# Kernel tuning notes

Measured on AMD Instinct MI355X. Metric: run time of the kernel, lower is better.

The kernel has to match this reference:

```python
import jax, jax.numpy as jnp
import numpy as np
import math

# Fixed ChunkedBlockDiagonalMask configuration (int metadata, closed over)
BATCH_SIZES = [32, 16, 8]
SEQ_LENS = [512, 1024, 2048]
NUM_HEADS = 8
HEAD_DIM = 64
TOTAL_TOKENS = sum(b * s for b, s in zip(BATCH_SIZES, SEQ_LENS))  # 49152


def setup_inputs() -> dict:
    key = jax.random.key(0)
    kq, kk, kv = jax.random.split(key, 3)
    shape = (1, NUM_HEADS, TOTAL_TOKENS, HEAD_DIM)
    return {
        "query": jax.random.normal(kq, shape, dtype=jnp.float32),
        "key": jax.random.normal(kk, shape, dtype=jnp.float32),
        "value": jax.random.normal(kv, shape, dtype=jnp.float32),
    }


def _sdpa(q, k, v):
    # q,k,v: [B, H, S, D]; native-backend math: softmax(q k^T / sqrt(D)) v
    scale = 1.0 / math.sqrt(q.shape[-1])
    scores = jnp.einsum("bhqd,bhkd->bhqk", q * scale, k)
    probs = jax.nn.softmax(scores, axis=-1)
    return jnp.einsum("bhqk,bhkd->bhqd", probs, v)


def reference(query, key, value):
    # Packed layout: [1, H, sum_i(B_i*S_i), D]; per-chunk token dim is (B_i S_i)
    H, D = query.shape[1], query.shape[3]
    outs = []
    offset = 0
    for b, s in zip(BATCH_SIZES, SEQ_LENS):
        n = b * s
        def unpack(t):
            # [1,H,(b s),D] -> [b,H,s,D]
            c = t[0, :, offset:offset + n, :]          # [H, b*s, D]
            return c.reshape(H, b, s, D).transpose(1, 0, 2, 3)
        o = _sdpa(unpack(query), unpack(key), unpack(value))  # [b,H,s,D]
        outs.append(o.transpose(1, 0, 2, 3).reshape(1, H, n, D))
        offset += n
    return jnp.concatenate(outs, axis=2)
```

## Files before the change

### kernel.cpp

```cpp
#include <hip/hip_runtime.h>

typedef __bf16 bf16_t;
typedef bf16_t bf16x8 __attribute__((ext_vector_type(8)));
typedef float f32x16 __attribute__((ext_vector_type(16)));
typedef unsigned short u16x8_t __attribute__((ext_vector_type(8)));
typedef unsigned int u32x4_t __attribute__((ext_vector_type(4)));

#define HD 64
#define TOTTOK 49152

static __device__ __forceinline__ unsigned short f2b(float f) {
    bf16_t h = (bf16_t)f;
    return __builtin_bit_cast(unsigned short, h);
}
static __device__ __forceinline__ bf16x8 asbf(u16x8_t u) { return __builtin_bit_cast(bf16x8, u); }
static __device__ __forceinline__ bf16x8 asbf4(u32x4_t u) { return __builtin_bit_cast(bf16x8, u); }
static __device__ __forceinline__ unsigned int pk2(float lo, float hi) {
    return (unsigned int)f2b(lo) | ((unsigned int)f2b(hi) << 16);
}

__global__ __launch_bounds__(256, 2)
void flash_attn_kernel(const float* __restrict__ Q, const float* __restrict__ K,
                       const float* __restrict__ V, float* __restrict__ O)
{
    __shared__ unsigned short Kf[2][4096];
    __shared__ unsigned short Vff[2][4096];

    const int bid = blockIdx.x;
    int Slen, bl2, off, qtl2, base;
    if (bid < 512)       { Slen = 2048; bl2 = 3; off = 32768; qtl2 = 3; base = 0;    }
    else if (bid < 1024) { Slen = 1024; bl2 = 4; off = 16384; qtl2 = 2; base = 512;  }
    else                 { Slen = 512;  bl2 = 5; off = 0;     qtl2 = 1; base = 1024; }
    const int l    = bid - base;
    const int xcd  = l & 7;
    const int slot = l >> 3;
    const int p    = xcd + ((slot >> qtl2) << 3);
    const int qblk = slot & ((1 << qtl2) - 1);
    const int hh   = p >> bl2;
    const int sj   = p & ((1 << bl2) - 1);

    const size_t seqbase = ((size_t)hh * TOTTOK + (size_t)off + (size_t)sj * Slen) * HD;
    const float* Qb = Q + seqbase + (size_t)(qblk * 256) * HD;
    const float* Kb = K + seqbase;
    const float* Vb = V + seqbase;
    float*       Ob = O + seqbase + (size_t)(qblk * 256) * HD;

    const int tid  = threadIdx.x;
    const int wave = tid >> 6;
    const int lane = tid & 63;
    const int l31  = lane & 31;
    const int hl   = lane >> 5;

    const float SC = 0.125f * 1.4426950408889634f;

    bf16x8 qf[2][4];
#pragma unroll
    for (int qt = 0; qt < 2; ++qt)
#pragma unroll
      for (int kk = 0; kk < 4; ++kk) {
        const float* src = Qb + (size_t)(wave*64 + qt*32 + l31) * HD + kk*16 + hl*8;
        float4 a = *(const float4*)src;
        float4 b = *(const float4*)(src + 4);
        float f[8] = {a.x,a.y,a.z,a.w,b.x,b.y,b.z,b.w};
        bf16x8 v;
#pragma unroll
        for (int i = 0; i < 8; ++i) v[i] = (bf16_t)(f[i] * SC);
        qf[qt][kk] = v;
      }

    f32x16 oacc[2][2];
    f32x16 lacc[2];
#pragma unroll
    for (int i = 0; i < 16; ++i) {
      oacc[0][0][i] = 0.f; oacc[0][1][i] = 0.f;
      oacc[1][0][i] = 0.f; oacc[1][1][i] = 0.f;
      lacc[0][i] = 0.f;    lacc[1][i] = 0.f;
    }

    u16x8_t onesu;
#pragma unroll
    for (int i = 0; i < 8; ++i) onesu[i] = 0x3F80;
    const bf16x8 ones = asbf(onesu);

    const int krow = tid & 31;
    const int kcol = ((tid >> 6) & 3) * 16 + ((tid >> 5) & 1) * 8;
    const int vkey = ((tid >> 6) & 3) * 16 + ((tid >> 5) & 1) * 8;
    const int vd   = tid & 31;

    float4 kr0, kr1, kr2, kr3;
    float vra[8], vrb[8];

    auto LOADT = [&](int it) {
      const float* Ksrc = Kb + (size_t)(it * 64) * HD;
      const float* Vsrc = Vb + (size_t)(it * 64) * HD;
      kr0 = *(const float4*)(Ksrc + (size_t)krow * HD + kcol);
      kr1 = *(const float4*)(Ksrc + (size_t)krow * HD + kcol + 4);
      kr2 = *(const float4*)(Ksrc + (size_t)(krow + 32) * HD + kcol);
      kr3 = *(const float4*)(Ksrc + (size_t)(krow + 32) * HD + kcol + 4);
#pragma unroll
      for (int i = 0; i < 8; ++i) {
        vra[i] = Vsrc[(size_t)(vkey + i) * HD + vd];
        vrb[i] = Vsrc[(size_t)(vkey + i) * HD + vd + 32];
      }
    };
    auto STORET = [&](int buf) {
      u16x8_t a;
      a[0]=f2b(kr0.x); a[1]=f2b(kr0.y); a[2]=f2b(kr0.z); a[3]=f2b(kr0.w);
      a[4]=f2b(kr1.x); a[5]=f2b(kr1.y); a[6]=f2b(kr1.z); a[7]=f2b(kr1.w);
      *(u16x8_t*)&Kf[buf][tid*8] = a;
      a[0]=f2b(kr2.x); a[1]=f2b(kr2.y); a[2]=f2b(kr2.z); a[3]=f2b(kr2.w);
      a[4]=f2b(kr3.x); a[5]=f2b(kr3.y); a[6]=f2b(kr3.z); a[7]=f2b(kr3.w);
      *(u16x8_t*)&Kf[buf][2048 + tid*8] = a;
      u16x8_t b;
#pragma unroll
      for (int i = 0; i < 8; ++i) b[i] = f2b(vra[i]);
      *(u16x8_t*)&Vff[buf][tid*8] = b;
#pragma unroll
      for (int i = 0; i < 8; ++i) b[i] = f2b(vrb[i]);
      *(u16x8_t*)&Vff[buf][2048 + tid*8] = b;
    };

    const int niter = Slen >> 6;
    LOADT(0);
    STORET(0);
    __syncthreads();

    for (int it = 0; it < niter; ++it) {
      const int cur = it & 1;
      const bool more = (it + 1 < niter);
      if (more) LOADT(it + 1);

      bf16x8 kf[8];
#pragma unroll
      for (int c2 = 0; c2 < 8; ++c2)
        kf[c2] = asbf(*(const u16x8_t*)&Kf[cur][c2*512 + lane*8]);

      u32x4_t pb[2][4];
#pragma unroll
      for (int qt = 0; qt < 2; ++qt) {
        f32x16 s0, s1;
#pragma unroll
        for (int i = 0; i < 16; ++i) { s0[i] = 0.f; s1[i] = 0.f; }
        __builtin_amdgcn_s_setprio(1);
#pragma unroll
        for (int kk = 0; kk < 4; ++kk) {
          s0 = __builtin_amdgcn_mfma_f32_32x32x16_bf16(kf[kk],     qf[qt][kk], s0, 0, 0, 0);
          s1 = __builtin_amdgcn_mfma_f32_32x32x16_bf16(kf[4 + kk], qf[qt][kk], s1, 0, 0, 0);
        }
        __builtin_amdgcn_s_setprio(0);
#pragma unroll
        for (int kt = 0; kt < 2; ++kt) {
          const f32x16& s = kt ? s1 : s0;
#pragma unroll
          for (int m = 0; m < 2; ++m) {
            unsigned int w0 = pk2(__builtin_amdgcn_exp2f(s[8*m+0]), __builtin_amdgcn_exp2f(s[8*m+1]));
            unsigned int w1 = pk2(__builtin_amdgcn_exp2f(s[8*m+2]), __builtin_amdgcn_exp2f(s[8*m+3]));
            unsigned int w2 = pk2(__builtin_amdgcn_exp2f(s[8*m+4]), __builtin_amdgcn_exp2f(s[8*m+5]));
            unsigned int w3 = pk2(__builtin_amdgcn_exp2f(s[8*m+6]), __builtin_amdgcn_exp2f(s[8*m+7]));
            asm("v_permlane32_swap_b32 %0, %1" : "+v"(w0), "+v"(w2));
            asm("v_permlane32_swap_b32 %0, %1" : "+v"(w1), "+v"(w3));
            pb[qt][2*kt + m] = (u32x4_t){w0, w1, w2, w3};
          }
        }
      }

      bf16x8 vf[8];
#pragma unroll
      for (int c2 = 0; c2 < 8; ++c2)
        vf[c2] = asbf(*(const u16x8_t*)&Vff[cur][c2*512 + lane*8]);

      __builtin_amdgcn_s_setprio(1);
#pragma unroll
      for (int kk4 = 0; kk4 < 4; ++kk4) {
        bf16x8 p0 = asbf4(pb[0][kk4]);
        bf16x8 p1 = asbf4(pb[1][kk4]);
        lacc[0] = __builtin_amdgcn_mfma_f32_32x32x16_bf16(ones, p0, lacc[0], 0, 0, 0);
        lacc[1] = __builtin_amdgcn_mfma_f32_32x32x16_bf16(ones, p1, lacc[1], 0, 0, 0);
        oacc[0][0] = __builtin_amdgcn_mfma_f32_32x32x16_bf16(vf[kk4],     p0, oacc[0][0], 0, 0, 0);
        oacc[0][1] = __builtin_amdgcn_mfma_f32_32x32x16_bf16(vf[kk4],     p1, oacc[0][1], 0, 0, 0);
        oacc[1][0] = __builtin_amdgcn_mfma_f32_32x32x16_bf16(vf[4 + kk4], p0, oacc[1][0], 0, 0, 0);
        oacc[1][1] = __builtin_amdgcn_mfma_f32_32x32x16_bf16(vf[4 + kk4], p1, oacc[1][1], 0, 0, 0);
      }
      __builtin_amdgcn_s_setprio(0);

      if (more) {
        STORET(cur ^ 1);
        __syncthreads();
      }
    }

#pragma unroll
    for (int qt = 0; qt < 2; ++qt) {
      float inv = 1.0f / lacc[qt][0];
      float* dst = Ob + (size_t)(wave*64 + qt*32 + l31) * HD + hl*4;
#pragma unroll
      for (int dt = 0; dt < 2; ++dt)
#pragma unroll
        for (int b = 0; b < 4; ++b) {
          float4 o4;
          o4.x = oacc[dt][qt][4*b+0] * inv;
          o4.y = oacc[dt][qt][4*b+1] * inv;
          o4.z = oacc[dt][qt][4*b+2] * inv;
          o4.w = oacc[dt][qt][4*b+3] * inv;
          *(float4*)(dst + dt*32 + b*8) = o4;
        }
    }
}

extern "C" void kernel_launch(void* const* d_in, const int* in_sizes, int n_in,
                              void* d_out, int out_size, void* d_ws, size_t ws_size,
                              hipStream_t stream) {
    (void)in_sizes; (void)n_in; (void)out_size; (void)d_ws; (void)ws_size;
    const float* Q = (const float*)d_in[0];
    const float* K = (const float*)d_in[1];
    const float* V = (const float*)d_in[2];
    float* O = (float*)d_out;
    flash_attn_kernel<<<dim3(1536), dim3(256), 0, stream>>>(Q, K, V, O);
}
```

Measured before the change: 198.4 us.

## Pipeline QK softmax with previous PV and compute row sums in VALU

Restructures the main loop so the QK^T and exp of the next key tile are issued alongside the PV MFMAs of the previous tile, using a triple-buffered V tile in shared memory. Row sums of the probabilities are accumulated in fp32 registers with one cross-half shuffle at the end, replacing the ones-vector MFMAs. This removes a third of the PV MFMAs and aims to overlap exp/VALU work with matrix work. It raises register pressure from the extra probability buffer and LDS use from the third V buffer. The sum now uses unrounded exps rather than the bf16 values used in PV.

```diff
diff --git a/kernel.cpp b/kernel.cpp
--- a/kernel.cpp
+++ b/kernel.cpp
@@ -24,7 +24,7 @@
                        const float* __restrict__ V, float* __restrict__ O)
 {
     __shared__ unsigned short Kf[2][4096];
-    __shared__ unsigned short Vff[2][4096];
+    __shared__ unsigned short Vff[3][4096];
 
     const int bid = blockIdx.x;
     int Slen, bl2, off, qtl2, base;
@@ -69,18 +69,12 @@
       }
 
     f32x16 oacc[2][2];
-    f32x16 lacc[2];
+    float lsum[2] = {0.f, 0.f};
 #pragma unroll
     for (int i = 0; i < 16; ++i) {
       oacc[0][0][i] = 0.f; oacc[0][1][i] = 0.f;
       oacc[1][0][i] = 0.f; oacc[1][1][i] = 0.f;
-      lacc[0][i] = 0.f;    lacc[1][i] = 0.f;
     }
-
-    u16x8_t onesu;
-#pragma unroll
-    for (int i = 0; i < 8; ++i) onesu[i] = 0x3F80;
-    const bf16x8 ones = asbf(onesu);
 
     const int krow = tid & 31;
     const int kcol = ((tid >> 6) & 3) * 16 + ((tid >> 5) & 1) * 8;
@@ -103,39 +97,32 @@
         vrb[i] = Vsrc[(size_t)(vkey + i) * HD + vd + 32];
       }
     };
-    auto STORET = [&](int buf) {
+    auto STORET = [&](int tile, int vbuf) {
+      unsigned short* kd = &Kf[tile & 1][0];
       u16x8_t a;
       a[0]=f2b(kr0.x); a[1]=f2b(kr0.y); a[2]=f2b(kr0.z); a[3]=f2b(kr0.w);
       a[4]=f2b(kr1.x); a[5]=f2b(kr1.y); a[6]=f2b(kr1.z); a[7]=f2b(kr1.w);
-      *(u16x8_t*)&Kf[buf][tid*8] = a;
+      *(u16x8_t*)(kd + tid*8) = a;
       a[0]=f2b(kr2.x); a[1]=f2b(kr2.y); a[2]=f2b(kr2.z); a[3]=f2b(kr2.w);
       a[4]=f2b(kr3.x); a[5]=f2b(kr3.y); a[6]=f2b(kr3.z); a[7]=f2b(kr3.w);
-      *(u16x8_t*)&Kf[buf][2048 + tid*8] = a;
+      *(u16x8_t*)(kd + 2048 + tid*8) = a;
+      unsigned short* vdst = &Vff[vbuf][0];
       u16x8_t b;
 #pragma unroll
       for (int i = 0; i < 8; ++i) b[i] = f2b(vra[i]);
-      *(u16x8_t*)&Vff[buf][tid*8] = b;
+      *(u16x8_t*)(vdst + tid*8) = b;
 #pragma unroll
       for (int i = 0; i < 8; ++i) b[i] = f2b(vrb[i]);
-      *(u16x8_t*)&Vff[buf][2048 + tid*8] = b;
-    };
-
-    const int niter = Slen >> 6;
-    LOADT(0);
-    STORET(0);
-    __syncthreads();
-
-    for (int it = 0; it < niter; ++it) {
-      const int cur = it & 1;
-      const bool more = (it + 1 < niter);
-      if (more) LOADT(it + 1);
-
+      *(u16x8_t*)(vdst + 2048 + tid*8) = b;
+    };
+
+    u32x4_t pbA[2][4], pbB[2][4];
+
+    auto QKS = [&](const unsigned short* kb, u32x4_t (&pbo)[2][4]) {
       bf16x8 kf[8];
 #pragma unroll
       for (int c2 = 0; c2 < 8; ++c2)
-        kf[c2] = asbf(*(const u16x8_t*)&Kf[cur][c2*512 + lane*8]);
-
-      u32x4_t pb[2][4];
+        kf[c2] = asbf(*(const u16x8_t*)(kb + c2*512 + lane*8));
 #pragma unroll
       for (int qt = 0; qt < 2; ++qt) {
         f32x16 s0, s1;
@@ -148,50 +135,81 @@
           s1 = __builtin_amdgcn_mfma_f32_32x32x16_bf16(kf[4 + kk], qf[qt][kk], s1, 0, 0, 0);
         }
         __builtin_amdgcn_s_setprio(0);
+        float ls = 0.f;
 #pragma unroll
         for (int kt = 0; kt < 2; ++kt) {
           const f32x16& s = kt ? s1 : s0;
 #pragma unroll
           for (int m = 0; m < 2; ++m) {
-            unsigned int w0 = pk2(__builtin_amdgcn_exp2f(s[8*m+0]), __builtin_amdgcn_exp2f(s[8*m+1]));
-            unsigned int w1 = pk2(__builtin_amdgcn_exp2f(s[8*m+2]), __builtin_amdgcn_exp2f(s[8*m+3]));
-            unsigned int w2 = pk2(__builtin_amdgcn_exp2f(s[8*m+4]), __builtin_amdgcn_exp2f(s[8*m+5]));
-            unsigned int w3 = pk2(__builtin_amdgcn_exp2f(s[8*m+6]), __builtin_amdgcn_exp2f(s[8*m+7]));
+            float e0 = __builtin_amdgcn_exp2f(s[8*m+0]), e1 = __builtin_amdgcn_exp2f(s[8*m+1]);
+            float e2 = __builtin_amdgcn_exp2f(s[8*m+2]), e3 = __builtin_amdgcn_exp2f(s[8*m+3]);
+            float e4 = __builtin_amdgcn_exp2f(s[8*m+4]), e5 = __builtin_amdgcn_exp2f(s[8*m+5]);
+            float e6 = __builtin_amdgcn_exp2f(s[8*m+6]), e7 = __builtin_amdgcn_exp2f(s[8*m+7]);
+            ls += ((e0 + e1) + (e2 + e3)) + ((e4 + e5) + (e6 + e7));
+            unsigned int w0 = pk2(e0, e1);
+            unsigned int w1 = pk2(e2, e3);
+            unsigned int w2 = pk2(e4, e5);
+            unsigned int w3 = pk2(e6, e7);
             asm("v_permlane32_swap_b32 %0, %1" : "+v"(w0), "+v"(w2));
             asm("v_permlane32_swap_b32 %0, %1" : "+v"(w1), "+v"(w3));
-            pb[qt][2*kt + m] = (u32x4_t){w0, w1, w2, w3};
+            pbo[qt][2*kt + m] = (u32x4_t){w0, w1, w2, w3};
           }
         }
-      }
-
-      bf16x8 vf[8];
-#pragma unroll
-      for (int c2 = 0; c2 < 8; ++c2)
-        vf[c2] = asbf(*(const u16x8_t*)&Vff[cur][c2*512 + lane*8]);
-
+        lsum[qt] += ls;
+      }
+    };
+
+    auto PV = [&](const u32x4_t (&pbi)[2][4], const unsigned short* vb) {
       __builtin_amdgcn_s_setprio(1);
 #pragma unroll
       for (int kk4 = 0; kk4 < 4; ++kk4) {
-        bf16x8 p0 = asbf4(pb[0][kk4]);
-        bf16x8 p1 = asbf4(pb[1][kk4]);
-        lacc[0] = __builtin_amdgcn_mfma_f32_32x32x16_bf16(ones, p0, lacc[0], 0, 0, 0);
-        lacc[1] = __builtin_amdgcn_mfma_f32_32x32x16_bf16(ones, p1, lacc[1], 0, 0, 0);
-        oacc[0][0] = __builtin_amdgcn_mfma_f32_32x32x16_bf16(vf[kk4],     p0, oacc[0][0], 0, 0, 0);
-        oacc[0][1] = __builtin_amdgcn_mfma_f32_32x32x16_bf16(vf[kk4],     p1, oacc[0][1], 0, 0, 0);
-        oacc[1][0] = __builtin_amdgcn_mfma_f32_32x32x16_bf16(vf[4 + kk4], p0, oacc[1][0], 0, 0, 0);
-        oacc[1][1] = __builtin_amdgcn_mfma_f32_32x32x16_bf16(vf[4 + kk4], p1, oacc[1][1], 0, 0, 0);
+        bf16x8 v0 = asbf(*(const u16x8_t*)(vb + kk4*512 + lane*8));
+        bf16x8 v1 = asbf(*(const u16x8_t*)(vb + (4 + kk4)*512 + lane*8));
+        bf16x8 p0 = asbf4(pbi[0][kk4]);
+        bf16x8 p1 = asbf4(pbi[1][kk4]);
+        oacc[0][0] = __builtin_amdgcn_mfma_f32_32x32x16_bf16(v0, p0, oacc[0][0], 0, 0, 0);
+        oacc[0][1] = __builtin_amdgcn_mfma_f32_32x32x16_bf16(v0, p1, oacc[0][1], 0, 0, 0);
+        oacc[1][0] = __builtin_amdgcn_mfma_f32_32x32x16_bf16(v1, p0, oacc[1][0], 0, 0, 0);
+        oacc[1][1] = __builtin_amdgcn_mfma_f32_32x32x16_bf16(v1, p1, oacc[1][1], 0, 0, 0);
       }
       __builtin_amdgcn_s_setprio(0);
-
+    };
+
+    const int niter = Slen >> 6;
+
+    LOADT(0);
+    STORET(0, 0);
+    __syncthreads();
+
+    LOADT(1);
+    QKS(&Kf[0][0], pbA);
+    STORET(1, 1);
+    __syncthreads();
+
+    int vprev = 0;
+    int vst   = 2;
+    for (int it = 1; it < niter; ++it) {
+      const bool more = (it + 1 < niter);
+      if (more) LOADT(it + 1);
+      PV(pbA, &Vff[vprev][0]);
+      QKS(&Kf[it & 1][0], pbB);
+#pragma unroll
+      for (int qt = 0; qt < 2; ++qt)
+#pragma unroll
+        for (int k = 0; k < 4; ++k) pbA[qt][k] = pbB[qt][k];
       if (more) {
-        STORET(cur ^ 1);
+        STORET(it + 1, vst);
         __syncthreads();
       }
+      vprev = (vprev == 2) ? 0 : vprev + 1;
+      vst   = (vst   == 2) ? 0 : vst   + 1;
     }
+    PV(pbA, &Vff[vprev][0]);
 
 #pragma unroll
     for (int qt = 0; qt < 2; ++qt) {
-      float inv = 1.0f / lacc[qt][0];
+      float ls = lsum[qt] + __shfl_xor(lsum[qt], 32);
+      float inv = 1.0f / ls;
       float* dst = Ob + (size_t)(wave*64 + qt*32 + l31) * HD + hl*4;
 #pragma unroll
       for (int dt = 0; dt < 2; ++dt)
```

After: 668.0 us. 3.37x slower.

## Process two 64-key tiles per barrier with split global loads

Applied to the files above, without the earlier changes.

The main loop now handles 128 keys per iteration, stored as two 64-key sub-tiles in each double-buffered LDS slot. The global loads for the next epoch are split so that each sub-tile's load is hidden behind one compute body, and there is one __syncthreads per 128 keys instead of per 64. V fragments are now read from LDS inside the PV MFMA loop instead of being preloaded, which lowers register pressure. The cost is twice the LDS footprint (32KB per block), which may affect occupancy at two blocks per CU, and a larger unrolled body.

```diff
diff --git a/kernel.cpp b/kernel.cpp
--- a/kernel.cpp
+++ b/kernel.cpp
@@ -19,12 +19,63 @@
     return (unsigned int)f2b(lo) | ((unsigned int)f2b(hi) << 16);
 }
 
+#define BODY(KBASE, VBASE)                                                             \
+  do {                                                                                 \
+    bf16x8 kf[8];                                                                      \
+    _Pragma("unroll")                                                                  \
+    for (int c2 = 0; c2 < 8; ++c2)                                                     \
+      kf[c2] = asbf(*(const u16x8_t*)((KBASE) + c2*512 + lane*8));                     \
+    u32x4_t pb[2][4];                                                                  \
+    _Pragma("unroll")                                                                  \
+    for (int qt = 0; qt < 2; ++qt) {                                                   \
+      f32x16 s0, s1;                                                                   \
+      _Pragma("unroll")                                                                \
+      for (int i = 0; i < 16; ++i) { s0[i] = 0.f; s1[i] = 0.f; }                       \
+      __builtin_amdgcn_s_setprio(1);                                                   \
+      _Pragma("unroll")                                                                \
+      for (int kk = 0; kk < 4; ++kk) {                                                 \
+        s0 = __builtin_amdgcn_mfma_f32_32x32x16_bf16(kf[kk],   qf[qt][kk], s0, 0, 0, 0); \
+        s1 = __builtin_amdgcn_mfma_f32_32x32x16_bf16(kf[4+kk], qf[qt][kk], s1, 0, 0, 0); \
+      }                                                                                \
+      __builtin_amdgcn_s_setprio(0);                                                   \
+      _Pragma("unroll")                                                                \
+      for (int kt = 0; kt < 2; ++kt) {                                                 \
+        const f32x16& s = kt ? s1 : s0;                                                \
+        _Pragma("unroll")                                                              \
+        for (int m = 0; m < 2; ++m) {                                                  \
+          unsigned int w0 = pk2(__builtin_amdgcn_exp2f(s[8*m+0]), __builtin_amdgcn_exp2f(s[8*m+1])); \
+          unsigned int w1 = pk2(__builtin_amdgcn_exp2f(s[8*m+2]), __builtin_amdgcn_exp2f(s[8*m+3])); \
+          unsigned int w2 = pk2(__builtin_amdgcn_exp2f(s[8*m+4]), __builtin_amdgcn_exp2f(s[8*m+5])); \
+          unsigned int w3 = pk2(__builtin_amdgcn_exp2f(s[8*m+6]), __builtin_amdgcn_exp2f(s[8*m+7])); \
+          asm("v_permlane32_swap_b32 %0, %1" : "+v"(w0), "+v"(w2));                    \
+          asm("v_permlane32_swap_b32 %0, %1" : "+v"(w1), "+v"(w3));                    \
+          pb[qt][2*kt + m] = (u32x4_t){w0, w1, w2, w3};                                \
+        }                                                                              \
+      }                                                                                \
+    }                                                                                  \
+    __builtin_amdgcn_s_setprio(1);                                                     \
+    _Pragma("unroll")                                                                  \
+    for (int kk4 = 0; kk4 < 4; ++kk4) {                                                \
+      bf16x8 v0 = asbf(*(const u16x8_t*)((VBASE) + kk4*512 + lane*8));                 \
+      bf16x8 v1 = asbf(*(const u16x8_t*)((VBASE) + (4+kk4)*512 + lane*8));             \
+      bf16x8 p0 = asbf4(pb[0][kk4]);                                                   \
+      bf16x8 p1 = asbf4(pb[1][kk4]);                                                   \
+      lacc[0] = __builtin_amdgcn_mfma_f32_32x32x16_bf16(ones, p0, lacc[0], 0, 0, 0);   \
+      lacc[1] = __builtin_amdgcn_mfma_f32_32x32x16_bf16(ones, p1, lacc[1], 0, 0, 0);   \
+      oacc[0][0] = __builtin_amdgcn_mfma_f32_32x32x16_bf16(v0, p0, oacc[0][0], 0, 0, 0); \
+      oacc[0][1] = __builtin_amdgcn_mfma_f32_32x32x16_bf16(v0, p1, oacc[0][1], 0, 0, 0); \
+      oacc[1][0] = __builtin_amdgcn_mfma_f32_32x32x16_bf16(v1, p0, oacc[1][0], 0, 0, 0); \
+      oacc[1][1] = __builtin_amdgcn_mfma_f32_32x32x16_bf16(v1, p1, oacc[1][1], 0, 0, 0); \
+    }                                                                                  \
+    __builtin_amdgcn_s_setprio(0);                                                     \
+  } while (0)
+
 __global__ __launch_bounds__(256, 2)
 void flash_attn_kernel(const float* __restrict__ Q, const float* __restrict__ K,
                        const float* __restrict__ V, float* __restrict__ O)
 {
-    __shared__ unsigned short Kf[2][4096];
-    __shared__ unsigned short Vff[2][4096];
+    __shared__ unsigned short Kf[2][2][4096];
+    __shared__ unsigned short Vff[2][2][4096];
 
     const int bid = blockIdx.x;
     int Slen, bl2, off, qtl2, base;
@@ -90,9 +141,9 @@
     float4 kr0, kr1, kr2, kr3;
     float vra[8], vrb[8];
 
-    auto LOADT = [&](int it) {
-      const float* Ksrc = Kb + (size_t)(it * 64) * HD;
-      const float* Vsrc = Vb + (size_t)(it * 64) * HD;
+    auto LOADT = [&](int keybase) {
+      const float* Ksrc = Kb + (size_t)keybase * HD;
+      const float* Vsrc = Vb + (size_t)keybase * HD;
       kr0 = *(const float4*)(Ksrc + (size_t)krow * HD + kcol);
       kr1 = *(const float4*)(Ksrc + (size_t)krow * HD + kcol + 4);
       kr2 = *(const float4*)(Ksrc + (size_t)(krow + 32) * HD + kcol);
@@ -103,88 +154,43 @@
         vrb[i] = Vsrc[(size_t)(vkey + i) * HD + vd + 32];
       }
     };
-    auto STORET = [&](int buf) {
+    auto STORET = [&](unsigned short* kdst, unsigned short* vdst) {
       u16x8_t a;
       a[0]=f2b(kr0.x); a[1]=f2b(kr0.y); a[2]=f2b(kr0.z); a[3]=f2b(kr0.w);
       a[4]=f2b(kr1.x); a[5]=f2b(kr1.y); a[6]=f2b(kr1.z); a[7]=f2b(kr1.w);
-      *(u16x8_t*)&Kf[buf][tid*8] = a;
+      *(u16x8_t*)(kdst + tid*8) = a;
       a[0]=f2b(kr2.x); a[1]=f2b(kr2.y); a[2]=f2b(kr2.z); a[3]=f2b(kr2.w);
       a[4]=f2b(kr3.x); a[5]=f2b(kr3.y); a[6]=f2b(kr3.z); a[7]=f2b(kr3.w);
-      *(u16x8_t*)&Kf[buf][2048 + tid*8] = a;
+      *(u16x8_t*)(kdst + 2048 + tid*8) = a;
       u16x8_t b;
 #pragma unroll
       for (int i = 0; i < 8; ++i) b[i] = f2b(vra[i]);
-      *(u16x8_t*)&Vff[buf][tid*8] = b;
+      *(u16x8_t*)(vdst + tid*8) = b;
 #pragma unroll
       for (int i = 0; i < 8; ++i) b[i] = f2b(vrb[i]);
-      *(u16x8_t*)&Vff[buf][2048 + tid*8] = b;
+      *(u16x8_t*)(vdst + 2048 + tid*8) = b;
     };
 
-    const int niter = Slen >> 6;
+    const int nep = Slen >> 7;
+
     LOADT(0);
-    STORET(0);
+    STORET(&Kf[0][0][0], &Vff[0][0][0]);
+    LOADT(64);
+    STORET(&Kf[0][1][0], &Vff[0][1][0]);
     __syncthreads();
 
-    for (int it = 0; it < niter; ++it) {
-      const int cur = it & 1;
-      const bool more = (it + 1 < niter);
-      if (more) LOADT(it + 1);
-
-      bf16x8 kf[8];
-#pragma unroll
-      for (int c2 = 0; c2 < 8; ++c2)
-        kf[c2] = asbf(*(const u16x8_t*)&Kf[cur][c2*512 + lane*8]);
-
-      u32x4_t pb[2][4];
-#pragma unroll
-      for (int qt = 0; qt < 2; ++qt) {
-        f32x16 s0, s1;
-#pragma unroll
-        for (int i = 0; i < 16; ++i) { s0[i] = 0.f; s1[i] = 0.f; }
-        __builtin_amdgcn_s_setprio(1);
-#pragma unroll
-        for (int kk = 0; kk < 4; ++kk) {
-          s0 = __builtin_amdgcn_mfma_f32_32x32x16_bf16(kf[kk],     qf[qt][kk], s0, 0, 0, 0);
-          s1 = __builtin_amdgcn_mfma_f32_32x32x16_bf16(kf[4 + kk], qf[qt][kk], s1, 0, 0, 0);
-        }
-        __builtin_amdgcn_s_setprio(0);
-#pragma unroll
-        for (int kt = 0; kt < 2; ++kt) {
-          const f32x16& s = kt ? s1 : s0;
-#pragma unroll
-          for (int m = 0; m < 2; ++m) {
-            unsigned int w0 = pk2(__builtin_amdgcn_exp2f(s[8*m+0]), __builtin_amdgcn_exp2f(s[8*m+1]));
-            unsigned int w1 = pk2(__builtin_amdgcn_exp2f(s[8*m+2]), __builtin_amdgcn_exp2f(s[8*m+3]));
-            unsigned int w2 = pk2(__builtin_amdgcn_exp2f(s[8*m+4]), __builtin_amdgcn_exp2f(s[8*m+5]));
-            unsigned int w3 = pk2(__builtin_amdgcn_exp2f(s[8*m+6]), __builtin_amdgcn_exp2f(s[8*m+7]));
-            asm("v_permlane32_swap_b32 %0, %1" : "+v"(w0), "+v"(w2));
-            asm("v_permlane32_swap_b32 %0, %1" : "+v"(w1), "+v"(w3));
-            pb[qt][2*kt + m] = (u32x4_t){w0, w1, w2, w3};
-          }
-        }
-      }
-
-      bf16x8 vf[8];
-#pragma unroll
-      for (int c2 = 0; c2 < 8; ++c2)
-        vf[c2] = asbf(*(const u16x8_t*)&Vff[cur][c2*512 + lane*8]);
-
-      __builtin_amdgcn_s_setprio(1);
-#pragma unroll
-      for (int kk4 = 0; kk4 < 4; ++kk4) {
-        bf16x8 p0 = asbf4(pb[0][kk4]);
-        bf16x8 p1 = asbf4(pb[1][kk4]);
-        lacc[0] = __builtin_amdgcn_mfma_f32_32x32x16_bf16(ones, p0, lacc[0], 0, 0, 0);
-        lacc[1] = __builtin_amdgcn_mfma_f32_32x32x16_bf16(ones, p1, lacc[1], 0, 0, 0);
-        oacc[0][0] = __builtin_amdgcn_mfma_f32_32x32x16_bf16(vf[kk4],     p0, oacc[0][0], 0, 0, 0);
-        oacc[0][1] = __builtin_amdgcn_mfma_f32_32x32x16_bf16(vf[kk4],     p1, oacc[0][1], 0, 0, 0);
-        oacc[1][0] = __builtin_amdgcn_mfma_f32_32x32x16_bf16(vf[4 + kk4], p0, oacc[1][0], 0, 0, 0);
-        oacc[1][1] = __builtin_amdgcn_mfma_f32_32x32x16_bf16(vf[4 + kk4], p1, oacc[1][1], 0, 0, 0);
-      }
-      __builtin_amdgcn_s_setprio(0);
-
+    for (int ep = 0; ep < nep; ++ep) {
+      const int cur = ep & 1;
+      const bool more = (ep + 1 < nep);
+      if (more) LOADT((ep + 1) * 128);
+      BODY(&Kf[cur][0][0], &Vff[cur][0][0]);
       if (more) {
-        STORET(cur ^ 1);
+        STORET(&Kf[cur ^ 1][0][0], &Vff[cur ^ 1][0][0]);
+        LOADT((ep + 1) * 128 + 64);
+      }
+      BODY(&Kf[cur][1][0], &Vff[cur][1][0]);
+      if (more) {
+        STORET(&Kf[cur ^ 1][1][0], &Vff[cur ^ 1][1][0]);
         __syncthreads();
       }
     }
```

Result: no change. 195.8 us (-1.3%).
